# Optimization experiments

Hardware: AMD Instinct MI355X
Metric: run time of the kernel (lower is better)

## Reference

```python
import jax, jax.numpy as jnp
import numpy as np

B, T, U = 4, 300, 100
D_E, D_P, D_MODEL, VOCAB = 512, 512, 512, 1024


def setup_inputs() -> dict:
    key = jax.random.key(0)
    ks = jax.random.split(key, 8)
    s = lambda d: 1.0 / np.sqrt(d)
    return {
        "encoder_outputs": jax.random.normal(ks[0], (B, T, D_E), jnp.float32),
        "predictor_outputs": jax.random.normal(ks[1], (B, U, D_P), jnp.float32),
        "W_enc": jax.random.normal(ks[2], (D_E, D_MODEL), jnp.float32) * s(D_E),
        "b_enc": jnp.zeros((D_MODEL,), jnp.float32),
        "W_pred": jax.random.normal(ks[3], (D_P, D_MODEL), jnp.float32) * s(D_P),
        "b_pred": jnp.zeros((D_MODEL,), jnp.float32),
        "W_joint": jax.random.normal(ks[4], (D_MODEL, VOCAB), jnp.float32) * s(D_MODEL),
        "b_joint": jnp.zeros((VOCAB,), jnp.float32),
    }


def reference(encoder_outputs, predictor_outputs, W_enc, b_enc, W_pred, b_pred, W_joint, b_joint):
    # f: [B, T, D], g: [B, U, D]
    f = jnp.einsum("bte,ed->btd", encoder_outputs, W_enc) + b_enc
    g = jnp.einsum("bup,pd->bud", predictor_outputs, W_pred) + b_pred
    # broadcast add -> [B, T, U, D], tanh activation
    joint_inputs = jnp.tanh(f[:, :, None, :] + g[:, None, :, :])
    # vocab projection -> [B, T, U, V]
    joint_outs = jnp.einsum("btud,dv->btuv", joint_inputs, W_joint) + b_joint
    return joint_outs
```

## Files before the change

kernel.cpp:

```cpp
#include <hip/hip_runtime.h>
#include <hip/hip_bf16.h>
#include <cstdint>


typedef __attribute__((ext_vector_type(4))) float f32x4;
typedef __attribute__((ext_vector_type(8))) short s16x8;

#define B_ 4
#define T_ 300
#define U_ 100
#define DM 512
#define VOC 1024
#define M_MAIN (B_*T_*U_)
#define M_MAIN_PAD 120064
#define M_ENC_PAD 1280
#define M_PRED_PAD 512

__device__ __forceinline__ unsigned short f2bf(float x) {
  unsigned int u = __builtin_bit_cast(unsigned int, x);
  u += 0x7FFFu + ((u >> 16) & 1u);
  return (unsigned short)(u >> 16);
}

__device__ __forceinline__ float fast_tanh(float x) {
  float e = __builtin_amdgcn_exp2f(x * 2.8853900817779268f);
  return fmaf(-2.0f, __builtin_amdgcn_rcpf(e + 1.0f), 1.0f);
}

__device__ __forceinline__ void gload_lds16(const void* g, void* l) {
  __builtin_amdgcn_global_load_lds(
      (const __attribute__((address_space(1))) void*)g,
      (__attribute__((address_space(3))) void*)l, 16, 0, 0);
}

__global__ void k_cvtpad(const float* __restrict__ enc, const float* __restrict__ pred,
                         unsigned short* __restrict__ encb, unsigned short* __restrict__ predb)
{
  int idx = blockIdx.x * 256 + threadIdx.x;
  const int encCh = M_ENC_PAD * 64;
  const float* src; unsigned short* dst; int Mv; int id2;
  if (idx < encCh) { src = enc; dst = encb; Mv = B_*T_; id2 = idx; }
  else            { id2 = idx - encCh; src = pred; dst = predb; Mv = B_*U_; }
  int r = id2 >> 6, k = (id2 & 63) * 8;
  s16x8 v;
  if (r < Mv) {
    f32x4 a = *(const f32x4*)(src + r*DM + k);
    f32x4 b = *(const f32x4*)(src + r*DM + k + 4);
#pragma unroll
    for (int j = 0; j < 4; ++j) { v[j] = (short)f2bf(a[j]); v[4+j] = (short)f2bf(b[j]); }
  } else {
#pragma unroll
    for (int j = 0; j < 8; ++j) v[j] = 0;
  }
  *(s16x8*)(dst + (long)id2 * 8) = v;
}

__global__ void k_transpose3(const float* __restrict__ We, const float* __restrict__ Wp,
                             const float* __restrict__ Wj,
                             unsigned short* __restrict__ WeT, unsigned short* __restrict__ WpT,
                             unsigned short* __restrict__ WjT)
{
  __shared__ float tile[32][33];
  const float* src; unsigned short* dst; int Ccols;
  const int R = 512;
  if (blockIdx.z == 0)      { src = We; dst = WeT; Ccols = 512; }
  else if (blockIdx.z == 1) { src = Wp; dst = WpT; Ccols = 512; }
  else                      { src = Wj; dst = WjT; Ccols = 1024; }
  int bx = blockIdx.x, by = blockIdx.y;
  if (bx * 32 >= Ccols) return;
  int x = threadIdx.x & 31, y = threadIdx.x >> 5;
  int c0 = bx * 32, r0 = by * 32;
#pragma unroll
  for (int i = 0; i < 4; ++i)
    tile[y + i*8][x] = src[(r0 + y + i*8) * Ccols + c0 + x];
  __syncthreads();
#pragma unroll
  for (int i = 0; i < 4; ++i)
    dst[(c0 + y + i*8) * R + r0 + x] = f2bf(tile[x][y + i*8]);
}

__device__ __forceinline__ void gemm_body(const unsigned short* __restrict__ A,
                                          const unsigned short* __restrict__ Bt,
                                          const float* __restrict__ bias,
                                          float* __restrict__ C,
                                          int Mvalid, int ldc, int mt, int nt)
{
  __shared__ unsigned short lza[128*64];
  __shared__ unsigned short lzb[128*64];
  const int tid  = threadIdx.x;
  const int wave = tid >> 6;
  const int lane = tid & 63;
  const int row0 = mt * 128;
  const int col0 = nt * 128;
  const int wm = (wave >> 1) * 64;
  const int wn = (wave & 1) * 64;

  const int rloc0 = wave*32 + (lane >> 3);
  const int srcc  = (lane & 7) ^ (rloc0 & 7);
  const unsigned short* gA = A  + (row0 + rloc0)*DM + srcc*8;
  const unsigned short* gB = Bt + (col0 + rloc0)*DM + srcc*8;
  unsigned short* ldsA = &lza[(wave*32)*64];
  unsigned short* ldsB = &lzb[(wave*32)*64];

  f32x4 acc[4][4] = {};

  for (int kt = 0; kt < DM/64; ++kt) {
    __syncthreads();
#pragma unroll
    for (int i = 0; i < 4; ++i) {
      gload_lds16(gA + i*8*DM, ldsA + i*8*64);
      gload_lds16(gB + i*8*DM, ldsB + i*8*64);
    }
    gA += 64; gB += 64;
    __syncthreads();
#pragma unroll
    for (int kk = 0; kk < 2; ++kk) {
      s16x8 af[4], bfr[4];
#pragma unroll
      for (int m = 0; m < 4; ++m) {
        int r = wm + m*16 + (lane & 15);
        int c = (kk*4 + (lane >> 4)) ^ (r & 7);
        af[m] = *(const s16x8*)&lza[r*64 + c*8];
      }
#pragma unroll
      for (int n = 0; n < 4; ++n) {
        int r = wn + n*16 + (lane & 15);
        int c = (kk*4 + (lane >> 4)) ^ (r & 7);
        bfr[n] = *(const s16x8*)&lzb[r*64 + c*8];
      }
#pragma unroll
      for (int m = 0; m < 4; ++m)
#pragma unroll
        for (int n = 0; n < 4; ++n)
          acc[m][n] = __builtin_amdgcn_mfma_f32_16x16x32_bf16(af[m], bfr[n], acc[m][n], 0, 0, 0);
    }
  }

  const int cl = lane & 15, rq = (lane >> 4) * 4;
#pragma unroll
  for (int n = 0; n < 4; ++n) {
    int col = col0 + wn + n*16 + cl;
    float bv = bias[col];
#pragma unroll
    for (int m = 0; m < 4; ++m) {
      int rb = row0 + wm + m*16 + rq;
#pragma unroll
      for (int j = 0; j < 4; ++j) {
        int r = rb + j;
        if (r < Mvalid) C[(long)r * ldc + col] = acc[m][n][j] + bv;
      }
    }
  }
}

__global__ __launch_bounds__(256, 2) void k_gemm_fg(
    const unsigned short* __restrict__ encb,  const unsigned short* __restrict__ WeT,
    const float* __restrict__ b_enc,  float* __restrict__ f,
    const unsigned short* __restrict__ predb, const unsigned short* __restrict__ WpT,
    const float* __restrict__ b_pred, float* __restrict__ g)
{
  const unsigned short* A;  const unsigned short* Bt;
  const float* bias; float* C; int Mv;
  if (blockIdx.z == 0) { A = encb;  Bt = WeT; bias = b_enc;  C = f; Mv = M_ENC_PAD; }
  else {
    if (blockIdx.x >= M_PRED_PAD/128) return;
    A = predb; Bt = WpT; bias = b_pred; C = g; Mv = M_PRED_PAD;
  }
  gemm_body(A, Bt, bias, C, Mv, DM, blockIdx.x, blockIdx.y);
}

__global__ void k_build_a(const float* __restrict__ f, const float* __restrict__ g,
                          unsigned short* __restrict__ Abuf)
{
  int idx = blockIdx.x * 256 + threadIdx.x;
  int r = idx >> 6;
  int k = (idx & 63) * 8;
  s16x8 v;
  if (r < M_MAIN) {
    int b   = r / (T_*U_);
    int rem = r - b * (T_*U_);
    int t   = rem / U_;
    int u   = rem - t * U_;
    const float* fr = f + (b*T_ + t) * DM + k;
    const float* gr = g + (b*U_ + u) * DM + k;
    f32x4 f0 = *(const f32x4*)fr;
    f32x4 f1 = *(const f32x4*)(fr + 4);
    f32x4 g0 = *(const f32x4*)gr;
    f32x4 g1 = *(const f32x4*)(gr + 4);
#pragma unroll
    for (int j = 0; j < 4; ++j) {
      v[j]   = (short)f2bf(fast_tanh(f0[j] + g0[j]));
      v[4+j] = (short)f2bf(fast_tanh(f1[j] + g1[j]));
    }
  } else {
#pragma unroll
    for (int j = 0; j < 8; ++j) v[j] = 0;
  }
  *(s16x8*)(Abuf + (long)idx * 8) = v;
}

__global__ __launch_bounds__(256, 2) void k_gemm_main(
    const unsigned short* __restrict__ A, const unsigned short* __restrict__ Bt,
    const float* __restrict__ bias, float* __restrict__ C)
{
  gemm_body(A, Bt, bias, C, M_MAIN, VOC, blockIdx.x, blockIdx.y);
}

extern "C" void kernel_launch(void* const* d_in, const int* in_sizes, int n_in,
                              void* d_out, int out_size, void* d_ws, size_t ws_size,
                              hipStream_t stream)
{
  const float* enc    = (const float*)d_in[0];
  const float* pred   = (const float*)d_in[1];
  const float* W_enc  = (const float*)d_in[2];
  const float* b_enc  = (const float*)d_in[3];
  const float* W_pred = (const float*)d_in[4];
  const float* b_pred = (const float*)d_in[5];
  const float* W_joint= (const float*)d_in[6];
  const float* b_joint= (const float*)d_in[7];
  float* out = (float*)d_out;

  char* w = (char*)d_ws;
  unsigned short* encb  = (unsigned short*)w; w += (long)M_ENC_PAD*DM*2;
  unsigned short* predb = (unsigned short*)w; w += (long)M_PRED_PAD*DM*2;
  unsigned short* WeT   = (unsigned short*)w; w += (long)DM*DM*2;
  unsigned short* WpT   = (unsigned short*)w; w += (long)DM*DM*2;
  unsigned short* WjT   = (unsigned short*)w; w += (long)VOC*DM*2;
  float*          f     = (float*)w;          w += (long)M_ENC_PAD*DM*4;
  float*          g     = (float*)w;          w += (long)M_PRED_PAD*DM*4;
  unsigned short* Abuf  = (unsigned short*)w; w += (long)M_MAIN_PAD*DM*2;

  k_cvtpad    <<<dim3(448),        dim3(256), 0, stream>>>(enc, pred, encb, predb);
  k_transpose3<<<dim3(32, 16, 3),  dim3(256), 0, stream>>>(W_enc, W_pred, W_joint, WeT, WpT, WjT);
  k_gemm_fg   <<<dim3(10, 4, 2),   dim3(256), 0, stream>>>(encb, WeT, b_enc, f, predb, WpT, b_pred, g);
  k_build_a   <<<dim3((M_MAIN_PAD*64)/256), dim3(256), 0, stream>>>(f, g, Abuf);
  k_gemm_main <<<dim3(938, 8),     dim3(256), 0, stream>>>(Abuf, WjT, b_joint, out);
}
```

Measured before the change: 350.7 us.

## Rewrite main GEMM with 256x256 tiles and 4-stage async LDS pipeline

Replaces the main vocab-projection GEMM with a 512-thread kernel using 256x256 output tiles and K-steps of 32. Global-to-LDS loads are issued three stages ahead into a four-buffer ring, with vmcnt waits and barriers in place of the load-then-sync loop. The larger tile raises reuse of the A and B operands, and the kernel adds priority hints around the MFMA block and nontemporal output stores. The costs are much higher register and LDS use (128 KB), lower occupancy, and a fragile hand-tuned wait-count schedule.

```diff
diff --git a/kernel.cpp b/kernel.cpp
--- a/kernel.cpp
+++ b/kernel.cpp
@@ -147,7 +147,7 @@
 #pragma unroll
       for (int j = 0; j < 4; ++j) {
         int r = rb + j;
-        if (r < Mvalid) C[(long)r * ldc + col] = acc[m][n][j] + bv;
+        if (r < Mvalid) __builtin_nontemporal_store(acc[m][n][j] + bv, &C[(long)r * ldc + col]);
       }
     }
   }
@@ -199,12 +199,107 @@
   *(s16x8*)(Abuf + (long)idx * 8) = v;
 }
 
-__global__ __launch_bounds__(256, 2) void k_gemm_main(
+#define WAITV(n) asm volatile("s_waitcnt vmcnt(" #n ")" ::: "memory")
+#define CFENCE   asm volatile("" ::: "memory")
+
+__global__ __launch_bounds__(512) void k_gemm_main(
     const unsigned short* __restrict__ A, const unsigned short* __restrict__ Bt,
     const float* __restrict__ bias, float* __restrict__ C)
 {
-  gemm_body(A, Bt, bias, C, M_MAIN, VOC, blockIdx.x, blockIdx.y);
-}
+  __shared__ unsigned short lds[65536];
+
+  const int bid = blockIdx.x;
+  const int mt = bid >> 2;
+  const int nt = bid & 3;
+  const int row0 = mt * 256;
+  const int col0 = nt * 256;
+
+  const int t = threadIdx.x;
+  const int w = t >> 6;
+  const int l = t & 63;
+  const int wm = w >> 2;
+  const int wn = w & 3;
+  const int lr = l & 15, lc = l >> 4;
+
+  const int sr = t >> 2;
+  const int scg = ((t & 3) - ((sr >> 1) & 3)) & 3;
+  const unsigned short* gA0 = A  + (long)(row0 +       sr) * DM + scg * 8;
+  const unsigned short* gA1 = A  + (long)(row0 + 128 + sr) * DM + scg * 8;
+  const unsigned short* gB0 = Bt + (long)(col0 +       sr) * DM + scg * 8;
+  const unsigned short* gB1 = Bt + (long)(col0 + 128 + sr) * DM + scg * 8;
+  const int dA = w * 512;
+
+#define STAGE(kt_) { const int bb = (kt_) & 3; \
+    gload_lds16(gA0 + (kt_)*32, &lds[bb*8192          + dA]); \
+    gload_lds16(gA1 + (kt_)*32, &lds[bb*8192 + 4096   + dA]); \
+    gload_lds16(gB0 + (kt_)*32, &lds[32768 + bb*8192        + dA]); \
+    gload_lds16(gB1 + (kt_)*32, &lds[32768 + bb*8192 + 4096 + dA]); }
+
+  int offA[8], offB[4];
+#pragma unroll
+  for (int m = 0; m < 8; ++m) {
+    int r = m*16 + lr;
+    offA[m] = wm*4096 + (r*4 + ((lc + (r>>1)) & 3)) * 8;
+  }
+#pragma unroll
+  for (int n = 0; n < 4; ++n) {
+    int cl2 = (wn & 1)*64 + n*16 + lr;
+    offB[n] = (wn >> 1)*4096 + (cl2*4 + ((lc + (cl2>>1)) & 3)) * 8;
+  }
+
+  f32x4 acc[8][4] = {};
+
+  STAGE(0); STAGE(1); STAGE(2);
+  WAITV(8);
+  __builtin_amdgcn_s_barrier();
+  CFENCE;
+
+#pragma unroll
+  for (int kt = 0; kt < 16; ++kt) {
+    const int b = kt & 3;
+    if (kt + 3 < 16) STAGE(kt + 3);
+
+    s16x8 af[8], bfv[4];
+#pragma unroll
+    for (int m = 0; m < 8; ++m) af[m] = *(const s16x8*)&lds[b*8192 + offA[m]];
+#pragma unroll
+    for (int n = 0; n < 4; ++n) bfv[n] = *(const s16x8*)&lds[32768 + b*8192 + offB[n]];
+
+    __builtin_amdgcn_s_setprio(1);
+#pragma unroll
+    for (int m = 0; m < 8; ++m)
+#pragma unroll
+      for (int n = 0; n < 4; ++n)
+        acc[m][n] = __builtin_amdgcn_mfma_f32_16x16x32_bf16(af[m], bfv[n], acc[m][n], 0, 0, 0);
+    __builtin_amdgcn_s_setprio(0);
+
+    if (kt < 15) {
+      if (kt <= 12)      WAITV(8);
+      else if (kt == 13) WAITV(4);
+      else               WAITV(0);
+      __builtin_amdgcn_s_barrier();
+      CFENCE;
+    }
+  }
+
+  const int rq = lc * 4;
+#pragma unroll
+  for (int n = 0; n < 4; ++n) {
+    int col = col0 + wn*64 + n*16 + lr;
+    float bv = bias[col];
+#pragma unroll
+    for (int m = 0; m < 8; ++m) {
+      int rb = row0 + wm*128 + m*16 + rq;
+#pragma unroll
+      for (int j = 0; j < 4; ++j) {
+        int r = rb + j;
+        if (r < M_MAIN)
+          __builtin_nontemporal_store(acc[m][n][j] + bv, &C[(long)r * VOC + col]);
+      }
+    }
+  }
+}
+#undef STAGE
 
 extern "C" void kernel_launch(void* const* d_in, const int* in_sizes, int n_in,
                               void* d_out, int out_size, void* d_ws, size_t ws_size,
@@ -234,5 +329,5 @@
   k_transpose3<<<dim3(32, 16, 3),  dim3(256), 0, stream>>>(W_enc, W_pred, W_joint, WeT, WpT, WjT);
   k_gemm_fg   <<<dim3(10, 4, 2),   dim3(256), 0, stream>>>(encb, WeT, b_enc, f, predb, WpT, b_pred, g);
   k_build_a   <<<dim3((M_MAIN_PAD*64)/256), dim3(256), 0, stream>>>(f, g, Abuf);
-  k_gemm_main <<<dim3(938, 8),     dim3(256), 0, stream>>>(Abuf, WjT, b_joint, out);
-}
+  k_gemm_main <<<dim3(469*4),      dim3(512), 0, stream>>>(Abuf, WjT, b_joint, out);
+}
```

Measured after the change: 308.5 us. 12.0% less time.

## Replace main GEMM with 256x256-tile, 8-wave double-buffered pipelined kernel

Applied to the files above, without the earlier changes.

Swaps the 128x128 single-buffered main GEMM for a 512-thread kernel with 256x256 output tiles. It double-buffers LDS and prefetches the next K-tile during MFMA phases, using explicit vmcnt waits, barriers and setprio. Output stores become nontemporal to avoid polluting cache with the large fp32 result. Larger tiles raise data reuse, but the kernel needs 128KB LDS and many accumulator registers, which limits occupancy and adds hand-tuned synchronization risk.

```diff
diff --git a/kernel.cpp b/kernel.cpp
--- a/kernel.cpp
+++ b/kernel.cpp
@@ -147,7 +147,7 @@
 #pragma unroll
       for (int j = 0; j < 4; ++j) {
         int r = rb + j;
-        if (r < Mvalid) C[(long)r * ldc + col] = acc[m][n][j] + bv;
+        if (r < Mvalid) __builtin_nontemporal_store(acc[m][n][j] + bv, &C[(long)r * ldc + col]);
       }
     }
   }
@@ -199,11 +199,128 @@
   *(s16x8*)(Abuf + (long)idx * 8) = v;
 }
 
-__global__ __launch_bounds__(256, 2) void k_gemm_main(
+__global__ __launch_bounds__(512, 2) void k_gemm_8p(
     const unsigned short* __restrict__ A, const unsigned short* __restrict__ Bt,
     const float* __restrict__ bias, float* __restrict__ C)
 {
-  gemm_body(A, Bt, bias, C, M_MAIN, VOC, blockIdx.x, blockIdx.y);
+  __shared__ unsigned short lds[65536];
+  char* ldsb = (char*)lds;
+
+  const int bid = blockIdx.x;
+  const int mt = bid >> 2, nt = bid & 3;
+  const long row0 = (long)mt * 256;
+  const int col0 = nt * 256;
+  const int t = threadIdx.x, w = t >> 6, l = t & 63;
+  const int rg = w >> 2;
+  const int cg = w & 3;
+  const int lr = l & 15, lc = l >> 4;
+
+  const int sr0 = w*16 + (l >> 3);
+  const int sr1 = sr0 + 8;
+  const int sc  = (l & 7) ^ (l >> 3);
+  const unsigned short* gp[4][2];
+  gp[0][0] = A  + (row0 +       sr0) * DM + sc*8;
+  gp[0][1] = A  + (row0 +       sr1) * DM + sc*8;
+  gp[3][0] = A  + (row0 + 128 + sr0) * DM + sc*8;
+  gp[3][1] = A  + (row0 + 128 + sr1) * DM + sc*8;
+  gp[1][0] = Bt + (long)(col0 +       sr0) * DM + sc*8;
+  gp[1][1] = Bt + (long)(col0 +       sr1) * DM + sc*8;
+  gp[2][0] = Bt + (long)(col0 + 128 + sr0) * DM + sc*8;
+  gp[2][1] = Bt + (long)(col0 + 128 + sr1) * DM + sc*8;
+  const int wbase = w * 2048;
+
+  int offA[4][2], offB[2][2];
+#pragma unroll
+  for (int q = 0; q < 4; ++q) {
+    int r = rg*64 + q*16 + lr;
+#pragma unroll
+    for (int kk = 0; kk < 2; ++kk)
+      offA[q][kk] = r*128 + (((kk*4 + lc) ^ (r & 7))*16);
+  }
+#pragma unroll
+  for (int j = 0; j < 2; ++j) {
+    int r = cg*32 + j*16 + lr;
+#pragma unroll
+    for (int kk = 0; kk < 2; ++kk)
+      offB[j][kk] = r*128 + (((kk*4 + lc) ^ (r & 7))*16);
+  }
+
+#define DO_STAGE(tile_, ty_) { \
+    const int dbase = (((ty_)==0 || (ty_)==3) ? 0 : 65536) + ((tile_)&1)*32768 \
+                      + (((ty_)>=2) ? 16384 : 0) + wbase; \
+    gload_lds16(gp[(ty_)][0] + (tile_)*64, ldsb + dbase); \
+    gload_lds16(gp[(ty_)][1] + (tile_)*64, ldsb + dbase + 1024); }
+
+#define PHASE(kt_, p_) { \
+    const int mp = (p_) >> 1, np = (p_) & 1; \
+    const int bufo = ((kt_) & 1) * 32768; \
+    if ((p_) == 0 && (kt_) < 7) { \
+      DO_STAGE((kt_)+1, 0); DO_STAGE((kt_)+1, 1); DO_STAGE((kt_)+1, 2); DO_STAGE((kt_)+1, 3); } \
+    s16x8 aq[4][2], bq[2][2]; \
+    _Pragma("unroll") \
+    for (int q = 0; q < 4; ++q) \
+      _Pragma("unroll") \
+      for (int kk = 0; kk < 2; ++kk) \
+        aq[q][kk] = *(const s16x8*)(ldsb + bufo + mp*16384 + offA[q][kk]); \
+    _Pragma("unroll") \
+    for (int j = 0; j < 2; ++j) \
+      _Pragma("unroll") \
+      for (int kk = 0; kk < 2; ++kk) \
+        bq[j][kk] = *(const s16x8*)(ldsb + 65536 + bufo + np*16384 + offB[j][kk]); \
+    if ((kt_) < 7) { \
+      if ((p_) == 0)      asm volatile("s_waitcnt vmcnt(10)" ::: "memory"); \
+      else if ((p_) == 1) asm volatile("s_waitcnt vmcnt(8)"  ::: "memory"); \
+      else if ((p_) == 3) asm volatile("s_waitcnt vmcnt(4)"  ::: "memory"); \
+    } else { \
+      if ((p_) == 0)      asm volatile("s_waitcnt vmcnt(2)"  ::: "memory"); \
+      else if ((p_) == 1) asm volatile("s_waitcnt vmcnt(0)"  ::: "memory"); \
+    } \
+    __builtin_amdgcn_s_barrier(); \
+    asm volatile("s_waitcnt lgkmcnt(0)" ::: "memory"); \
+    __builtin_amdgcn_sched_barrier(0); \
+    __builtin_amdgcn_s_setprio(1); \
+    _Pragma("unroll") \
+    for (int q = 0; q < 4; ++q) \
+      _Pragma("unroll") \
+      for (int j = 0; j < 2; ++j) \
+        _Pragma("unroll") \
+        for (int kk = 0; kk < 2; ++kk) \
+          acc[mp*4+q][np*2+j] = __builtin_amdgcn_mfma_f32_16x16x32_bf16( \
+              aq[q][kk], bq[j][kk], acc[mp*4+q][np*2+j], 0, 0, 0); \
+    __builtin_amdgcn_s_setprio(0); \
+    __builtin_amdgcn_s_barrier(); }
+
+  f32x4 acc[8][4] = {};
+
+  DO_STAGE(0, 0); DO_STAGE(0, 1); DO_STAGE(0, 2); DO_STAGE(0, 3);
+  asm volatile("s_waitcnt vmcnt(4)" ::: "memory");
+  __builtin_amdgcn_s_barrier();
+
+#pragma unroll
+  for (int kt = 0; kt < 8; ++kt) {
+    PHASE(kt, 0); PHASE(kt, 1); PHASE(kt, 2); PHASE(kt, 3);
+  }
+
+  const int rq = lc * 4;
+#pragma unroll
+  for (int n = 0; n < 4; ++n) {
+    const int np = n >> 1, j = n & 1;
+    int col = col0 + np*128 + cg*32 + j*16 + lr;
+    float bv = bias[col];
+#pragma unroll
+    for (int m = 0; m < 8; ++m) {
+      const int mp = m >> 2, q = m & 3;
+      long rb = row0 + mp*128 + rg*64 + q*16 + rq;
+#pragma unroll
+      for (int jj = 0; jj < 4; ++jj) {
+        long r = rb + jj;
+        if (r < M_MAIN)
+          __builtin_nontemporal_store(acc[m][n][jj] + bv, &C[r * VOC + col]);
+      }
+    }
+  }
+#undef DO_STAGE
+#undef PHASE
 }
 
 extern "C" void kernel_launch(void* const* d_in, const int* in_sizes, int n_in,
@@ -234,5 +351,5 @@
   k_transpose3<<<dim3(32, 16, 3),  dim3(256), 0, stream>>>(W_enc, W_pred, W_joint, WeT, WpT, WjT);
   k_gemm_fg   <<<dim3(10, 4, 2),   dim3(256), 0, stream>>>(encb, WeT, b_enc, f, predb, WpT, b_pred, g);
   k_build_a   <<<dim3((M_MAIN_PAD*64)/256), dim3(256), 0, stream>>>(f, g, Abuf);
-  k_gemm_main <<<dim3(938, 8),     dim3(256), 0, stream>>>(Abuf, WjT, b_joint, out);
-}
+  k_gemm_8p   <<<dim3(469*4),      dim3(512), 0, stream>>>(Abuf, WjT, b_joint, out);
+}
```

Result: faster. 321.4 us (-8.4%).

## Double-buffer main GEMM LDS loads with XCD-aware tile mapping and nontemporal stores

Applied to the files above, without the earlier changes.

Replaces the main vocab GEMM with a kernel that double-buffers LDS tiles, issuing global-to-LDS loads for the next K step while MFMAs run on the current one. It uses a single fused sync per step and raises wave priority around the MFMA block. Block IDs are remapped so each group of eight consecutive blocks spreads across M ranges, likely to keep row tiles local to an XCD's L2. Output stores become nontemporal to avoid polluting cache with the large write stream. Doubling LDS to 64KB per block may reduce occupancy.

```diff
diff --git a/kernel.cpp b/kernel.cpp
--- a/kernel.cpp
+++ b/kernel.cpp
@@ -147,7 +147,7 @@
 #pragma unroll
       for (int j = 0; j < 4; ++j) {
         int r = rb + j;
-        if (r < Mvalid) C[(long)r * ldc + col] = acc[m][n][j] + bv;
+        if (r < Mvalid) __builtin_nontemporal_store(acc[m][n][j] + bv, &C[(long)r * ldc + col]);
       }
     }
   }
@@ -199,11 +199,111 @@
   *(s16x8*)(Abuf + (long)idx * 8) = v;
 }
 
-__global__ __launch_bounds__(256, 2) void k_gemm_main(
+__global__ __launch_bounds__(256, 2) void k_gemm_2p(
     const unsigned short* __restrict__ A, const unsigned short* __restrict__ Bt,
     const float* __restrict__ bias, float* __restrict__ C)
 {
-  gemm_body(A, Bt, bias, C, M_MAIN, VOC, blockIdx.x, blockIdx.y);
+  __shared__ unsigned short lds[32768];
+  char* ldsb = (char*)lds;
+
+  const int bid = blockIdx.x;
+  const int x = bid & 7;
+  const int kq = bid >> 3;
+  const int ip = kq >> 3;
+  const int nt = kq & 7;
+  const int cnt = (x < 2) ? 118 : 117;
+  if (ip >= cnt) return;
+  const int mt = (x < 2) ? x*118 + ip : 236 + (x - 2)*117 + ip;
+  const long row0 = (long)mt * 128;
+  const int col0 = nt * 128;
+
+  const int t = threadIdx.x, w = t >> 6, l = t & 63;
+  const int wm = w >> 1, wn = w & 1, lr = l & 15, lc = l >> 4;
+
+  const int srl = w*8 + (l >> 3);
+  const int sc  = (l & 7) ^ (l >> 3);
+  const unsigned short* pA = A  + (row0 + srl) * DM + sc*8;
+  const unsigned short* pB = Bt + (long)(col0 + srl) * DM + sc*8;
+  const int wbase = w * 1024;
+
+#define STAGE(kt_, b_) { \
+    _Pragma("unroll") \
+    for (int s = 0; s < 4; ++s) \
+      gload_lds16(pA + (long)s*32*DM + (kt_)*64, ldsb + (b_)*32768 + s*4096 + wbase); \
+    _Pragma("unroll") \
+    for (int s = 0; s < 4; ++s) \
+      gload_lds16(pB + (long)s*32*DM + (kt_)*64, ldsb + (b_)*32768 + 16384 + s*4096 + wbase); }
+
+  int offA[4][2], offB[4][2];
+#pragma unroll
+  for (int m = 0; m < 4; ++m) {
+    int r = wm*64 + m*16 + lr;
+#pragma unroll
+    for (int kk = 0; kk < 2; ++kk)
+      offA[m][kk] = r*128 + (((kk*4 + lc) ^ (r & 7))*16);
+  }
+#pragma unroll
+  for (int n = 0; n < 4; ++n) {
+    int r = wn*64 + n*16 + lr;
+#pragma unroll
+    for (int kk = 0; kk < 2; ++kk)
+      offB[n][kk] = r*128 + (((kk*4 + lc) ^ (r & 7))*16);
+  }
+
+  f32x4 acc[4][4] = {};
+
+  STAGE(0, 0); STAGE(1, 1);
+  asm volatile("s_waitcnt vmcnt(8)" ::: "memory");
+  __builtin_amdgcn_s_barrier();
+
+#pragma unroll
+  for (int kt = 0; kt < 8; ++kt) {
+    const int cur = kt & 1;
+    if (kt >= 1 && kt < 7) STAGE(kt + 1, cur ^ 1);
+
+    s16x8 af[4][2], bf[4][2];
+#pragma unroll
+    for (int m = 0; m < 4; ++m)
+#pragma unroll
+      for (int kk = 0; kk < 2; ++kk)
+        af[m][kk] = *(const s16x8*)(ldsb + cur*32768 + offA[m][kk]);
+#pragma unroll
+    for (int n = 0; n < 4; ++n)
+#pragma unroll
+      for (int kk = 0; kk < 2; ++kk)
+        bf[n][kk] = *(const s16x8*)(ldsb + cur*32768 + 16384 + offB[n][kk]);
+
+    __builtin_amdgcn_s_setprio(1);
+#pragma unroll
+    for (int m = 0; m < 4; ++m)
+#pragma unroll
+      for (int n = 0; n < 4; ++n)
+#pragma unroll
+        for (int kk = 0; kk < 2; ++kk)
+          acc[m][n] = __builtin_amdgcn_mfma_f32_16x16x32_bf16(
+              af[m][kk], bf[n][kk], acc[m][n], 0, 0, 0);
+    __builtin_amdgcn_s_setprio(0);
+
+    if (kt < 7) __syncthreads();
+  }
+
+  const int rq = lc * 4;
+#pragma unroll
+  for (int n = 0; n < 4; ++n) {
+    int col = col0 + wn*64 + n*16 + lr;
+    float bv = bias[col];
+#pragma unroll
+    for (int m = 0; m < 4; ++m) {
+      long rb = row0 + wm*64 + m*16 + rq;
+#pragma unroll
+      for (int jj = 0; jj < 4; ++jj) {
+        long r = rb + jj;
+        if (r < M_MAIN)
+          __builtin_nontemporal_store(acc[m][n][jj] + bv, &C[r * VOC + col]);
+      }
+    }
+  }
+#undef STAGE
 }
 
 extern "C" void kernel_launch(void* const* d_in, const int* in_sizes, int n_in,
@@ -234,5 +334,5 @@
   k_transpose3<<<dim3(32, 16, 3),  dim3(256), 0, stream>>>(W_enc, W_pred, W_joint, WeT, WpT, WjT);
   k_gemm_fg   <<<dim3(10, 4, 2),   dim3(256), 0, stream>>>(encb, WeT, b_enc, f, predb, WpT, b_pred, g);
   k_build_a   <<<dim3((M_MAIN_PAD*64)/256), dim3(256), 0, stream>>>(f, g, Abuf);
-  k_gemm_main <<<dim3(938, 8),     dim3(256), 0, stream>>>(Abuf, WjT, b_joint, out);
-}
+  k_gemm_2p   <<<dim3(944*8),      dim3(256), 0, stream>>>(Abuf, WjT, b_joint, out);
+}
```

New measurement: 295.0 us. -15.9%, faster.
